# Optimization experiments

Hardware: AMD Instinct MI355X
Metric: run time of the kernel (lower is better)

The kernel has to match this reference:

```python
import jax, jax.numpy as jnp
import numpy as np

NUM_BINS = 10
HIST_RANGE = 10.0
LN_EPS = 1e-5
NUM_SERVERS = 64
START_IDX = 2 + 2 + NUM_SERVERS  # = 68


def layer_norm(x, g, b):
    mu = jnp.mean(x, axis=-1, keepdims=True)
    var = jnp.mean(jnp.square(x - mu), axis=-1, keepdims=True)
    return (x - mu) * jax.lax.rsqrt(var + LN_EPS) * g + b


def batched_histogram(w):
    # w: [B, S]; replicates np.histogram(w_i, bins=10, range=(0,10)) per row,
    # then normalizes by (sum + 1e-8). Values outside [0,10] are excluded;
    # value == 10 falls in the last bin.
    idx = jnp.clip(jnp.floor(w * (NUM_BINS / HIST_RANGE)).astype(jnp.int32), 0, NUM_BINS - 1)
    mask = ((w >= 0.0) & (w <= HIST_RANGE)).astype(w.dtype)
    oh = jax.nn.one_hot(idx, NUM_BINS, dtype=w.dtype) * mask[..., None]  # [B,S,NB]
    hist = jnp.sum(oh, axis=1)  # [B,NB]
    return hist / (jnp.sum(hist, axis=-1, keepdims=True) + 1e-8)


def setup_inputs() -> dict:
    key = jax.random.key(0)
    ks = jax.random.split(key, 16)
    B, OBS, ACT, H, NB = 65536, 512, 64, 128, NUM_BINS
    COMB = (OBS - NUM_SERVERS) + 128 + 64  # 640

    def lin(k, fin, fout):
        bound = 1.0 / np.sqrt(fin)
        kw, kb = jax.random.split(k)
        return (jax.random.uniform(kw, (fin, fout), jnp.float32, -bound, bound),
                jax.random.uniform(kb, (fout,), jnp.float32, -bound, bound))

    obs = jax.random.uniform(ks[0], (B, OBS), jnp.float32, 0.0, 10.0)
    preference = jax.random.uniform(ks[1], (B, 2), jnp.float32)
    h_w1, h_b1 = lin(ks[2], NB, H)
    h_w2, h_b2 = lin(ks[3], H, H)
    p_w, p_b = lin(ks[4], 2, 64)
    s_w1, s_b1 = lin(ks[5], COMB, 256)
    s_w2, s_b2 = lin(ks[6], 256, 256)
    qd_w, qd_b = lin(ks[7], 256, ACT)
    qe_w, qe_b = lin(ks[8], 256, ACT)
    return {
        'obs': obs, 'preference': preference,
        'h_w1': h_w1, 'h_b1': h_b1,
        'h_ln1_g': jnp.ones((H,)), 'h_ln1_b': jnp.zeros((H,)),
        'h_w2': h_w2, 'h_b2': h_b2,
        'h_ln2_g': jnp.ones((H,)), 'h_ln2_b': jnp.zeros((H,)),
        'p_w': p_w, 'p_b': p_b,
        'p_ln_g': jnp.ones((64,)), 'p_ln_b': jnp.zeros((64,)),
        's_w1': s_w1, 's_b1': s_b1,
        's_ln1_g': jnp.ones((256,)), 's_ln1_b': jnp.zeros((256,)),
        's_w2': s_w2, 's_b2': s_b2,
        's_ln2_g': jnp.ones((256,)), 's_ln2_b': jnp.zeros((256,)),
        'qd_w': qd_w, 'qd_b': qd_b, 'qe_w': qe_w, 'qe_b': qe_b,
    }


def reference(obs, preference,
              h_w1, h_b1, h_ln1_g, h_ln1_b, h_w2, h_b2, h_ln2_g, h_ln2_b,
              p_w, p_b, p_ln_g, p_ln_b,
              s_w1, s_b1, s_ln1_g, s_ln1_b, s_w2, s_b2, s_ln2_g, s_ln2_b,
              qd_w, qd_b, qe_w, qe_b):
    server_workloads = obs[:, START_IDX:START_IDX + NUM_SERVERS]
    obs_wo = jnp.concatenate([obs[:, :START_IDX], obs[:, START_IDX + NUM_SERVERS:]], axis=-1)

    hist = batched_histogram(server_workloads)  # [B, 10]
    h = layer_norm(jax.nn.relu(hist @ h_w1 + h_b1), h_ln1_g, h_ln1_b)
    h = layer_norm(jax.nn.relu(h @ h_w2 + h_b2), h_ln2_g, h_ln2_b)  # [B,128]

    p = layer_norm(jax.nn.relu(preference @ p_w + p_b), p_ln_g, p_ln_b)  # [B,64]

    combined = jnp.concatenate([obs_wo, h, p], axis=-1)  # [B,640]
    s = layer_norm(jax.nn.relu(combined @ s_w1 + s_b1), s_ln1_g, s_ln1_b)
    s = layer_norm(jax.nn.relu(s @ s_w2 + s_b2), s_ln2_g, s_ln2_b)  # [B,256]

    q_delay = s @ qd_w + qd_b   # [B,A]
    q_energy = s @ qe_w + qe_b  # [B,A]
    return jnp.stack([q_delay, q_energy], axis=-1)  # [B,A,2]
```

## Files before the change

kernel.cpp:

```cpp
#include <hip/hip_runtime.h>

typedef __bf16 bf16x8 __attribute__((ext_vector_type(8)));
typedef __bf16 bf16x4 __attribute__((ext_vector_type(4)));
typedef float  f32x4  __attribute__((ext_vector_type(4)));

#define OFF_W1  0
#define OFF_W2  163840
#define OFF_WQ  229376
#define OFF_WH1 262144
#define OFF_WH2 266240
#define WS_ELEMS 282624
#define CE_CH2 0
#define CE_EH2 128
#define CE_C2  256
#define CE_E2  512
#define CE_CQ  768
#define CE_EQ  896

__global__ __launch_bounds__(256) void prep_kernel(
    const float* __restrict__ s_w1, const float* __restrict__ s_w2,
    const float* __restrict__ qd_w, const float* __restrict__ qe_w,
    const float* __restrict__ h_w1, const float* __restrict__ h_w2,
    const float* __restrict__ h_g1, const float* __restrict__ s_g1,
    const float* __restrict__ s_g2,
    __bf16* __restrict__ wsb)
{
  int idx = blockIdx.x * 256 + threadIdx.x;
  if (idx >= WS_ELEMS) return;
  float val = 0.f;
  if (idx < OFF_W2) {
    int t = idx;
    int j = t & 7, l = (t >> 3) & 63, rest = t >> 9;
    int nt = rest & 15, ks = rest >> 4;
    int k = ks * 32 + (l >> 4) * 8 + j, n = nt * 16 + (l & 15);
    val = s_w1[k * 256 + n];
  } else if (idx < OFF_WQ) {
    int t = idx - OFF_W2;
    int j = t & 7, l = (t >> 3) & 63, rest = t >> 9;
    int nt = rest & 15, ks = rest >> 4;
    int k = ks * 32 + (l >> 4) * 8 + j, n = nt * 16 + (l & 15);
    val = s_w2[k * 256 + n] * s_g1[k];
  } else if (idx < OFF_WH1) {
    int t = idx - OFF_WQ;
    int j = t & 7, l = (t >> 3) & 63, rest = t >> 9;
    int nt = rest & 7, ks = rest >> 3;
    int k = ks * 32 + (l >> 4) * 8 + j, n = nt * 16 + (l & 15);
    int a = n >> 1;
    val = ((n & 1) ? qe_w[k * 64 + a] : qd_w[k * 64 + a]) * s_g2[k];
  } else if (idx < OFF_WH2) {
    int t = idx - OFF_WH1;
    int j = t & 7, l = (t >> 3) & 63, rest = t >> 9;
    int nt = rest & 7;
    int k = (l >> 4) * 8 + j, n = nt * 16 + (l & 15);
    val = (k < 10) ? h_w1[k * 128 + n] : 0.f;
  } else {
    int t = idx - OFF_WH2;
    int j = t & 7, l = (t >> 3) & 63, rest = t >> 9;
    int nt = rest & 7, ks = rest >> 3;
    int k = ks * 32 + (l >> 4) * 8 + j, n = nt * 16 + (l & 15);
    val = h_w2[k * 128 + n] * h_g1[k];
  }
  wsb[idx] = (__bf16)val;
}

__global__ __launch_bounds__(256) void prep_ce(
    const float* __restrict__ h_w2, const float* __restrict__ h_g1,
    const float* __restrict__ h_bb1, const float* __restrict__ h_b2,
    const float* __restrict__ s_w2, const float* __restrict__ s_g1,
    const float* __restrict__ s_bb1, const float* __restrict__ s_b2,
    const float* __restrict__ qd_w, const float* __restrict__ qe_w,
    const float* __restrict__ s_g2, const float* __restrict__ s_bb2,
    const float* __restrict__ qd_b, const float* __restrict__ qe_b,
    float* __restrict__ ce)
{
  int t = blockIdx.x * 256 + threadIdx.x;
  if (t < 128) {
    float s = 0.f;
    for (int k = 0; k < 128; ++k) s += h_g1[k] * h_w2[k * 128 + t];
    ce[CE_CH2 + t] = s;
  } else if (t < 256) {
    int n = t - 128;
    float s = h_b2[n];
    for (int k = 0; k < 128; ++k) s += h_bb1[k] * h_w2[k * 128 + n];
    ce[t] = s;
  } else if (t < 512) {
    int n = t - 256;
    float s = 0.f;
    for (int k = 0; k < 256; ++k) s += s_g1[k] * s_w2[k * 256 + n];
    ce[t] = s;
  } else if (t < 768) {
    int n = t - 512;
    float s = s_b2[n];
    for (int k = 0; k < 256; ++k) s += s_bb1[k] * s_w2[k * 256 + n];
    ce[t] = s;
  } else if (t < 896) {
    int n = t - 768, a = n >> 1;
    const float* W = (n & 1) ? qe_w : qd_w;
    float s = 0.f;
    for (int k = 0; k < 256; ++k) s += s_g2[k] * W[k * 64 + a];
    ce[t] = s;
  } else if (t < 1024) {
    int n = t - 896, a = n >> 1;
    const float* W = (n & 1) ? qe_w : qd_w;
    float s = (n & 1) ? qe_b[a] : qd_b[a];
    for (int k = 0; k < 256; ++k) s += s_bb2[k] * W[k * 64 + a];
    ce[t] = s;
  }
}

template<int CTRL>
__device__ __forceinline__ float dppadd(float x) {
  int p = __builtin_amdgcn_mov_dpp(__float_as_int(x), CTRL, 0xF, 0xF, true);
  return x + __int_as_float(p);
}
__device__ __forceinline__ float row16_reduce(float x) {
  x = dppadd<0x121>(x);
  x = dppadd<0x122>(x);
  x = dppadd<0x124>(x);
  x = dppadd<0x128>(x);
  return x;
}

__device__ __forceinline__ void slot_stats(const float* slot, float invW, int quad,
                                           float mu[4], float rs[4]) {
  f32x4 v0 = *(const f32x4*)(slot + quad * 8);
  f32x4 v1 = *(const f32x4*)(slot + quad * 8 + 4);
  float ts[4] = {v0[0], v0[2], v1[0], v1[2]};
  float tq[4] = {v0[1], v0[3], v1[1], v1[3]};
#pragma unroll
  for (int r = 0; r < 4; ++r) {
    mu[r] = ts[r] * invW;
    float var = tq[r] * invW - mu[r] * mu[r];
    rs[r] = rsqrtf(var + 1e-5f);
  }
}

template<int NTW>
__device__ __forceinline__ void reduce_slot(float x[NTW][4], float* slot, int lane) {
  const int quad = lane >> 4, ln = lane & 15;
  float s[4] = {0, 0, 0, 0}, q[4] = {0, 0, 0, 0};
#pragma unroll
  for (int i = 0; i < NTW; ++i)
#pragma unroll
    for (int r = 0; r < 4; ++r) { s[r] += x[i][r]; q[r] += x[i][r] * x[i][r]; }
#pragma unroll
  for (int r = 0; r < 4; ++r) { s[r] = row16_reduce(s[r]); q[r] = row16_reduce(q[r]); }
  if (ln == 0) {
#pragma unroll
    for (int r = 0; r < 4; ++r) {
      int m = quad * 4 + r;
      atomicAdd(&slot[2 * m], s[r]);
      atomicAdd(&slot[2 * m + 1], q[r]);
    }
  }
  __syncthreads();
}

template<int KSTEPS, int NT_TOT, int NTW>
__device__ __forceinline__ void run_gemm(const __bf16* A, int astride,
    const bf16x8* __restrict__ Bsw, int wave, int lane, f32x4 acc[NTW])
{
  const int quad = lane >> 4, ln = lane & 15;
  const int ntb = wave * NTW;
  bf16x8 bcur[NTW];
#pragma unroll
  for (int i = 0; i < NTW; ++i) bcur[i] = Bsw[(ntb + i) * 64 + lane];
#pragma unroll
  for (int ks = 0; ks < KSTEPS; ++ks) {
    bf16x8 bnxt[NTW];
    if (ks + 1 < KSTEPS) {
#pragma unroll
      for (int i = 0; i < NTW; ++i)
        bnxt[i] = Bsw[((ks + 1) * NT_TOT + ntb + i) * 64 + lane];
    }
    bf16x8 a = *(const bf16x8*)(A + ln * astride + ks * 32 + quad * 8);
#pragma unroll
    for (int i = 0; i < NTW; ++i)
      acc[i] = __builtin_amdgcn_mfma_f32_16x16x32_bf16(a, bcur[i], acc[i], 0, 0, 0);
    if (ks + 1 < KSTEPS) {
#pragma unroll
      for (int i = 0; i < NTW; ++i) bcur[i] = bnxt[i];
    }
  }
}

template<int NTW>
__device__ __forceinline__ void epilogue_raw(f32x4 acc[NTW],
    const float* __restrict__ bias,
    __bf16* Adst, int dstride, int dstcol0,
    float* slot, int wave, int lane)
{
  const int quad = lane >> 4, ln = lane & 15;
  float x[NTW][4];
#pragma unroll
  for (int i = 0; i < NTW; ++i) {
    int n = (wave * NTW + i) * 16 + ln;
    float b = bias[n];
#pragma unroll
    for (int r = 0; r < 4; ++r) {
      x[i][r] = fmaxf(acc[i][r] + b, 0.f);
      Adst[(quad * 4 + r) * dstride + dstcol0 + n] = (__bf16)x[i][r];
    }
  }
  reduce_slot<NTW>(x, slot, lane);
}

template<int NTW>
__device__ __forceinline__ void epilogue_fold_raw(f32x4 acc[NTW],
    const float* __restrict__ cvec, const float* __restrict__ evec,
    const float* __restrict__ slot_prev, float invWprev,
    __bf16* Adst, int dstride, int dstcol0,
    float* slot, int wave, int lane)
{
  const int quad = lane >> 4, ln = lane & 15;
  float mu[4], rs[4];
  slot_stats(slot_prev, invWprev, quad, mu, rs);
  float x[NTW][4];
#pragma unroll
  for (int i = 0; i < NTW; ++i) {
    int n = (wave * NTW + i) * 16 + ln;
    float c = cvec[n], e = evec[n];
#pragma unroll
    for (int r = 0; r < 4; ++r) {
      float z = fmaf(rs[r], fmaf(-mu[r], c, acc[i][r]), e);
      x[i][r] = fmaxf(z, 0.f);
      Adst[(quad * 4 + r) * dstride + dstcol0 + n] = (__bf16)x[i][r];
    }
  }
  reduce_slot<NTW>(x, slot, lane);
}

__global__ __launch_bounds__(512, 8) void critic_kernel(
    const float* __restrict__ obs, const float* __restrict__ pref,
    const float* __restrict__ h_b1,
    const float* __restrict__ h_g2, const float* __restrict__ h_bb2,
    const float* __restrict__ p_w, const float* __restrict__ p_b,
    const float* __restrict__ p_g, const float* __restrict__ p_bb,
    const float* __restrict__ s_b1,
    const __bf16* __restrict__ wsb, const float* __restrict__ ce,
    float* __restrict__ out)
{
  __shared__ __align__(16) __bf16 A_comb[16 * 648];
  __shared__ __align__(16) __bf16 A_s[16 * 264];
  __shared__ __align__(16) __bf16 A_h[16 * 40];
  __shared__ __align__(16) float red4[4][32];

  const int tid = threadIdx.x;
  const int wave = tid >> 6, lane = tid & 63;
  const int rowbase = blockIdx.x * 16;
  __bf16* X2 = A_comb;

  if (tid < 128) ((float*)red4)[tid] = 0.f;

  float pw0 = p_w[lane], pw1 = p_w[64 + lane], pb = p_b[lane];
  float pg = p_g[lane], pbb = p_bb[lane];
#pragma unroll
  for (int r = 0; r < 2; ++r) {
    int row = wave * 2 + r;
    int grow = rowbase + row;
    const float* orow = obs + (size_t)grow * 512;
#pragma unroll
    for (int j = 0; j < 2; ++j) {
      int l = lane + 64 * j;
      if (l < 112) {
        int src4 = (l < 17) ? l : l + 16;
        float4 v = *(const float4*)(orow + 4 * src4);
        bf16x4 o;
        o[0] = (__bf16)v.x; o[1] = (__bf16)v.y; o[2] = (__bf16)v.z; o[3] = (__bf16)v.w;
        *(bf16x4*)(&A_comb[row * 648 + 4 * l]) = o;
      }
    }
    float w = orow[68 + lane];
    int bi = (int)floorf(w);
    bi = bi < 0 ? 0 : (bi > 9 ? 9 : bi);
    bool valid = (w >= 0.f) && (w <= 10.f);
    float tot = 0.f, mine = 0.f;
#pragma unroll
    for (int b = 0; b < 10; ++b) {
      unsigned long long mk = __ballot(valid && (bi == b));
      float c = (float)__popcll(mk);
      tot += c;
      if (lane == b) mine = c;
    }
    float inv = 1.f / (tot + 1e-8f);
    if (lane < 32) A_h[row * 40 + lane] = (__bf16)((lane < 10) ? mine * inv : 0.f);
    float a0 = pref[grow * 2], a1 = pref[grow * 2 + 1];
    float v = fmaxf(fmaf(a0, pw0, fmaf(a1, pw1, pb)), 0.f);
    float s1 = v, s2 = v * v;
    s1 = row16_reduce(s1); s2 = row16_reduce(s2);
    s1 += __shfl_xor(s1, 16, 64); s2 += __shfl_xor(s2, 16, 64);
    s1 += __shfl_xor(s1, 32, 64); s2 += __shfl_xor(s2, 32, 64);
    float mu = s1 * (1.f / 64.f);
    float var = s2 * (1.f / 64.f) - mu * mu;
    float o = (v - mu) * rsqrtf(var + 1e-5f) * pg + pbb;
    A_comb[row * 648 + 576 + lane] = (__bf16)o;
  }
  __syncthreads();

  {
    f32x4 acc[1] = {};
    run_gemm<1, 8, 1>(A_h, 40, (const bf16x8*)(wsb + OFF_WH1), wave, lane, acc);
    epilogue_raw<1>(acc, h_b1, A_s, 264, 0, red4[0], wave, lane);
  }
  {
    f32x4 acc[1] = {};
    run_gemm<4, 8, 1>(A_s, 264, (const bf16x8*)(wsb + OFF_WH2), wave, lane, acc);
    const int quad = lane >> 4, ln = lane & 15;
    float mu0[4], rs0[4];
    slot_stats(red4[0], 1.f / 128.f, quad, mu0, rs0);
    int n = wave * 16 + ln;
    float c = ce[CE_CH2 + n], e = ce[CE_EH2 + n];
    float x[1][4];
#pragma unroll
    for (int r = 0; r < 4; ++r) {
      float z = fmaf(rs0[r], fmaf(-mu0[r], c, acc[0][r]), e);
      x[0][r] = fmaxf(z, 0.f);
    }
    reduce_slot<1>(x, red4[1], lane);
    float mu[4], rs[4];
    slot_stats(red4[1], 1.f / 128.f, quad, mu, rs);
    float gg = h_g2[n], bv = h_bb2[n];
#pragma unroll
    for (int r = 0; r < 4; ++r) {
      float o = (x[0][r] - mu[r]) * rs[r] * gg + bv;
      A_comb[(quad * 4 + r) * 648 + 448 + n] = (__bf16)o;
    }
    __syncthreads();
  }
  {
    f32x4 acc[2] = {};
    run_gemm<20, 16, 2>(A_comb, 648, (const bf16x8*)(wsb + OFF_W1), wave, lane, acc);
    epilogue_raw<2>(acc, s_b1, A_s, 264, 0, red4[2], wave, lane);
  }
  {
    f32x4 acc[2] = {};
    run_gemm<8, 16, 2>(A_s, 264, (const bf16x8*)(wsb + OFF_W2), wave, lane, acc);
    epilogue_fold_raw<2>(acc, ce + CE_C2, ce + CE_E2, red4[2], 1.f / 256.f,
                         X2, 264, 0, red4[3], wave, lane);
  }
  {
    f32x4 acc[1] = {};
    run_gemm<8, 8, 1>(X2, 264, (const bf16x8*)(wsb + OFF_WQ), wave, lane, acc);
    const int quad = lane >> 4, ln = lane & 15;
    float mu[4], rs[4];
    slot_stats(red4[3], 1.f / 256.f, quad, mu, rs);
    int n = wave * 16 + ln;
    float c = ce[CE_CQ + n], e = ce[CE_EQ + n];
#pragma unroll
    for (int r = 0; r < 4; ++r) {
      int m = quad * 4 + r;
      out[(size_t)(rowbase + m) * 128 + n] = fmaf(rs[r], fmaf(-mu[r], c, acc[0][r]), e);
    }
  }
}

extern "C" void kernel_launch(void* const* d_in, const int* in_sizes, int n_in,
                              void* d_out, int out_size, void* d_ws, size_t ws_size,
                              hipStream_t stream) {
  const float* obs    = (const float*)d_in[0];
  const float* pref   = (const float*)d_in[1];
  const float* h_w1   = (const float*)d_in[2];
  const float* h_b1   = (const float*)d_in[3];
  const float* h_g1   = (const float*)d_in[4];
  const float* h_bb1  = (const float*)d_in[5];
  const float* h_w2   = (const float*)d_in[6];
  const float* h_b2   = (const float*)d_in[7];
  const float* h_g2   = (const float*)d_in[8];
  const float* h_bb2  = (const float*)d_in[9];
  const float* p_w    = (const float*)d_in[10];
  const float* p_b    = (const float*)d_in[11];
  const float* p_g    = (const float*)d_in[12];
  const float* p_bb   = (const float*)d_in[13];
  const float* s_w1   = (const float*)d_in[14];
  const float* s_b1   = (const float*)d_in[15];
  const float* s_g1   = (const float*)d_in[16];
  const float* s_bb1  = (const float*)d_in[17];
  const float* s_w2   = (const float*)d_in[18];
  const float* s_b2   = (const float*)d_in[19];
  const float* s_g2   = (const float*)d_in[20];
  const float* s_bb2  = (const float*)d_in[21];
  const float* qd_w   = (const float*)d_in[22];
  const float* qd_b   = (const float*)d_in[23];
  const float* qe_w   = (const float*)d_in[24];
  const float* qe_b   = (const float*)d_in[25];

  __bf16* wsb = (__bf16*)d_ws;
  float* ce = (float*)(wsb + WS_ELEMS);
  int B = in_sizes[0] / 512;
  int nblocks = B / 16;

  prep_kernel<<<(WS_ELEMS + 255) / 256, 256, 0, stream>>>(
      s_w1, s_w2, qd_w, qe_w, h_w1, h_w2, h_g1, s_g1, s_g2, wsb);
  prep_ce<<<4, 256, 0, stream>>>(
      h_w2, h_g1, h_bb1, h_b2, s_w2, s_g1, s_bb1, s_b2,
      qd_w, qe_w, s_g2, s_bb2, qd_b, qe_b, ce);
  critic_kernel<<<nblocks, 512, 0, stream>>>(
      obs, pref, h_b1, h_g2, h_bb2, p_w, p_b, p_g, p_bb, s_b1,
      (const __bf16*)wsb, (const float*)ce, (float*)d_out);
}
```

Before: 346.5 us.

## Fold histogram LayerNorm2 into first trunk GEMM and merge prep kernels

Writes the un-normalised hidden activations straight into the combined buffer and folds the second histogram LayerNorm's gamma into the s_w1 rows. Its mean, rstd and beta are applied in the first trunk epilogue through precomputed column vectors, with the GEMM split into three K ranges so the hist segment gets its own accumulator. This removes a stats pass, a normalise-and-store pass and one __syncthreads. The two prep kernels are merged into one launch, and stats computation is hoisted before each GEMM. A barrier is dropped and floorf is replaced with truncation, which relies on the mask for negative values. The extra accumulators add register pressure.

```diff
diff --git a/kernel.cpp b/kernel.cpp
--- a/kernel.cpp
+++ b/kernel.cpp
@@ -16,17 +16,71 @@
 #define CE_E2  512
 #define CE_CQ  768
 #define CE_EQ  896
+#define CE_C1S 1024
+#define CE_E1S 1280
+#define CE_N   1536
 
 __global__ __launch_bounds__(256) void prep_kernel(
-    const float* __restrict__ s_w1, const float* __restrict__ s_w2,
+    const float* __restrict__ s_w1, const float* __restrict__ s_b1,
+    const float* __restrict__ s_w2, const float* __restrict__ s_b2,
     const float* __restrict__ qd_w, const float* __restrict__ qe_w,
+    const float* __restrict__ qd_b, const float* __restrict__ qe_b,
     const float* __restrict__ h_w1, const float* __restrict__ h_w2,
-    const float* __restrict__ h_g1, const float* __restrict__ s_g1,
-    const float* __restrict__ s_g2,
-    __bf16* __restrict__ wsb)
+    const float* __restrict__ h_b2,
+    const float* __restrict__ h_g1, const float* __restrict__ h_bb1,
+    const float* __restrict__ h_g2, const float* __restrict__ h_bb2,
+    const float* __restrict__ s_g1, const float* __restrict__ s_bb1,
+    const float* __restrict__ s_g2, const float* __restrict__ s_bb2,
+    __bf16* __restrict__ wsb, float* __restrict__ ce)
 {
   int idx = blockIdx.x * 256 + threadIdx.x;
-  if (idx >= WS_ELEMS) return;
+  if (idx >= WS_ELEMS) {
+    int t = idx - WS_ELEMS;
+    if (t >= CE_N) return;
+    if (t < 128) {
+      float s = 0.f;
+      for (int k = 0; k < 128; ++k) s += h_g1[k] * h_w2[k * 128 + t];
+      ce[CE_CH2 + t] = s;
+    } else if (t < 256) {
+      int n = t - 128;
+      float s = h_b2[n];
+      for (int k = 0; k < 128; ++k) s += h_bb1[k] * h_w2[k * 128 + n];
+      ce[t] = s;
+    } else if (t < 512) {
+      int n = t - 256;
+      float s = 0.f;
+      for (int k = 0; k < 256; ++k) s += s_g1[k] * s_w2[k * 256 + n];
+      ce[t] = s;
+    } else if (t < 768) {
+      int n = t - 512;
+      float s = s_b2[n];
+      for (int k = 0; k < 256; ++k) s += s_bb1[k] * s_w2[k * 256 + n];
+      ce[t] = s;
+    } else if (t < 896) {
+      int n = t - 768, a = n >> 1;
+      const float* W = (n & 1) ? qe_w : qd_w;
+      float s = 0.f;
+      for (int k = 0; k < 256; ++k) s += s_g2[k] * W[k * 64 + a];
+      ce[t] = s;
+    } else if (t < 1024) {
+      int n = t - 896, a = n >> 1;
+      const float* W = (n & 1) ? qe_w : qd_w;
+      float s = (n & 1) ? qe_b[a] : qd_b[a];
+      for (int k = 0; k < 256; ++k) s += s_bb2[k] * W[k * 64 + a];
+      ce[t] = s;
+    } else if (t < 1280) {
+      int n = t - 1024;
+      float s = 0.f;
+      for (int k = 0; k < 128; ++k) s += h_g2[k] * s_w1[(448 + k) * 256 + n];
+      ce[t] = s;
+    } else {
+      int n = t - 1280;
+      float s = s_b1[n];
+      for (int k = 0; k < 128; ++k) s += h_bb2[k] * s_w1[(448 + k) * 256 + n];
+      ce[t] = s;
+    }
+    return;
+  }
   float val = 0.f;
   if (idx < OFF_W2) {
     int t = idx;
@@ -34,6 +88,7 @@
     int nt = rest & 15, ks = rest >> 4;
     int k = ks * 32 + (l >> 4) * 8 + j, n = nt * 16 + (l & 15);
     val = s_w1[k * 256 + n];
+    if (k >= 448 && k < 576) val *= h_g2[k - 448];
   } else if (idx < OFF_WQ) {
     int t = idx - OFF_W2;
     int j = t & 7, l = (t >> 3) & 63, rest = t >> 9;
@@ -63,51 +118,6 @@
   wsb[idx] = (__bf16)val;
 }
 
-__global__ __launch_bounds__(256) void prep_ce(
-    const float* __restrict__ h_w2, const float* __restrict__ h_g1,
-    const float* __restrict__ h_bb1, const float* __restrict__ h_b2,
-    const float* __restrict__ s_w2, const float* __restrict__ s_g1,
-    const float* __restrict__ s_bb1, const float* __restrict__ s_b2,
-    const float* __restrict__ qd_w, const float* __restrict__ qe_w,
-    const float* __restrict__ s_g2, const float* __restrict__ s_bb2,
-    const float* __restrict__ qd_b, const float* __restrict__ qe_b,
-    float* __restrict__ ce)
-{
-  int t = blockIdx.x * 256 + threadIdx.x;
-  if (t < 128) {
-    float s = 0.f;
-    for (int k = 0; k < 128; ++k) s += h_g1[k] * h_w2[k * 128 + t];
-    ce[CE_CH2 + t] = s;
-  } else if (t < 256) {
-    int n = t - 128;
-    float s = h_b2[n];
-    for (int k = 0; k < 128; ++k) s += h_bb1[k] * h_w2[k * 128 + n];
-    ce[t] = s;
-  } else if (t < 512) {
-    int n = t - 256;
-    float s = 0.f;
-    for (int k = 0; k < 256; ++k) s += s_g1[k] * s_w2[k * 256 + n];
-    ce[t] = s;
-  } else if (t < 768) {
-    int n = t - 512;
-    float s = s_b2[n];
-    for (int k = 0; k < 256; ++k) s += s_bb1[k] * s_w2[k * 256 + n];
-    ce[t] = s;
-  } else if (t < 896) {
-    int n = t - 768, a = n >> 1;
-    const float* W = (n & 1) ? qe_w : qd_w;
-    float s = 0.f;
-    for (int k = 0; k < 256; ++k) s += s_g2[k] * W[k * 64 + a];
-    ce[t] = s;
-  } else if (t < 1024) {
-    int n = t - 896, a = n >> 1;
-    const float* W = (n & 1) ? qe_w : qd_w;
-    float s = (n & 1) ? qe_b[a] : qd_b[a];
-    for (int k = 0; k < 256; ++k) s += s_bb2[k] * W[k * 64 + a];
-    ce[t] = s;
-  }
-}
-
 template<int CTRL>
 __device__ __forceinline__ float dppadd(float x) {
   int p = __builtin_amdgcn_mov_dpp(__float_as_int(x), CTRL, 0xF, 0xF, true);
@@ -205,38 +215,11 @@
   reduce_slot<NTW>(x, slot, lane);
 }
 
-template<int NTW>
-__device__ __forceinline__ void epilogue_fold_raw(f32x4 acc[NTW],
-    const float* __restrict__ cvec, const float* __restrict__ evec,
-    const float* __restrict__ slot_prev, float invWprev,
-    __bf16* Adst, int dstride, int dstcol0,
-    float* slot, int wave, int lane)
-{
-  const int quad = lane >> 4, ln = lane & 15;
-  float mu[4], rs[4];
-  slot_stats(slot_prev, invWprev, quad, mu, rs);
-  float x[NTW][4];
-#pragma unroll
-  for (int i = 0; i < NTW; ++i) {
-    int n = (wave * NTW + i) * 16 + ln;
-    float c = cvec[n], e = evec[n];
-#pragma unroll
-    for (int r = 0; r < 4; ++r) {
-      float z = fmaf(rs[r], fmaf(-mu[r], c, acc[i][r]), e);
-      x[i][r] = fmaxf(z, 0.f);
-      Adst[(quad * 4 + r) * dstride + dstcol0 + n] = (__bf16)x[i][r];
-    }
-  }
-  reduce_slot<NTW>(x, slot, lane);
-}
-
 __global__ __launch_bounds__(512, 8) void critic_kernel(
     const float* __restrict__ obs, const float* __restrict__ pref,
     const float* __restrict__ h_b1,
-    const float* __restrict__ h_g2, const float* __restrict__ h_bb2,
     const float* __restrict__ p_w, const float* __restrict__ p_b,
     const float* __restrict__ p_g, const float* __restrict__ p_bb,
-    const float* __restrict__ s_b1,
     const __bf16* __restrict__ wsb, const float* __restrict__ ce,
     float* __restrict__ out)
 {
@@ -247,6 +230,7 @@
 
   const int tid = threadIdx.x;
   const int wave = tid >> 6, lane = tid & 63;
+  const int quad = lane >> 4, ln = lane & 15;
   const int rowbase = blockIdx.x * 16;
   __bf16* X2 = A_comb;
 
@@ -271,7 +255,7 @@
       }
     }
     float w = orow[68 + lane];
-    int bi = (int)floorf(w);
+    int bi = (int)w;
     bi = bi < 0 ? 0 : (bi > 9 ? 9 : bi);
     bool valid = (w >= 0.f) && (w <= 10.f);
     float tot = 0.f, mine = 0.f;
@@ -303,11 +287,10 @@
     epilogue_raw<1>(acc, h_b1, A_s, 264, 0, red4[0], wave, lane);
   }
   {
+    float mu0[4], rs0[4];
+    slot_stats(red4[0], 1.f / 128.f, quad, mu0, rs0);
     f32x4 acc[1] = {};
     run_gemm<4, 8, 1>(A_s, 264, (const bf16x8*)(wsb + OFF_WH2), wave, lane, acc);
-    const int quad = lane >> 4, ln = lane & 15;
-    float mu0[4], rs0[4];
-    slot_stats(red4[0], 1.f / 128.f, quad, mu0, rs0);
     int n = wave * 16 + ln;
     float c = ce[CE_CH2 + n], e = ce[CE_EH2 + n];
     float x[1][4];
@@ -315,41 +298,64 @@
     for (int r = 0; r < 4; ++r) {
       float z = fmaf(rs0[r], fmaf(-mu0[r], c, acc[0][r]), e);
       x[0][r] = fmaxf(z, 0.f);
+      A_comb[(quad * 4 + r) * 648 + 448 + n] = (__bf16)x[0][r];
     }
     reduce_slot<1>(x, red4[1], lane);
-    float mu[4], rs[4];
-    slot_stats(red4[1], 1.f / 128.f, quad, mu, rs);
-    float gg = h_g2[n], bv = h_bb2[n];
-#pragma unroll
-    for (int r = 0; r < 4; ++r) {
-      float o = (x[0][r] - mu[r]) * rs[r] * gg + bv;
-      A_comb[(quad * 4 + r) * 648 + 448 + n] = (__bf16)o;
-    }
-    __syncthreads();
   }
   {
-    f32x4 acc[2] = {};
-    run_gemm<20, 16, 2>(A_comb, 648, (const bf16x8*)(wsb + OFF_W1), wave, lane, acc);
-    epilogue_raw<2>(acc, s_b1, A_s, 264, 0, red4[2], wave, lane);
+    float mu1[4], rs1[4];
+    slot_stats(red4[1], 1.f / 128.f, quad, mu1, rs1);
+    const bf16x8* B1 = (const bf16x8*)(wsb + OFF_W1);
+    f32x4 accM[2] = {};
+    f32x4 accS[2] = {};
+    run_gemm<14, 16, 2>(A_comb, 648, B1, wave, lane, accM);
+    run_gemm<4, 16, 2>(A_comb + 448, 648, B1 + 14 * 16 * 64, wave, lane, accS);
+    run_gemm<2, 16, 2>(A_comb + 576, 648, B1 + 18 * 16 * 64, wave, lane, accM);
+    float x[2][4];
+#pragma unroll
+    for (int i = 0; i < 2; ++i) {
+      int n = (wave * 2 + i) * 16 + ln;
+      float c = ce[CE_C1S + n], e = ce[CE_E1S + n];
+#pragma unroll
+      for (int r = 0; r < 4; ++r) {
+        float t = fmaf(-mu1[r] * rs1[r], c, e);
+        float z = accM[i][r] + fmaf(rs1[r], accS[i][r], t);
+        x[i][r] = fmaxf(z, 0.f);
+        A_s[(quad * 4 + r) * 264 + n] = (__bf16)x[i][r];
+      }
+    }
+    reduce_slot<2>(x, red4[2], lane);
   }
   {
+    float mu2[4], rs2[4];
+    slot_stats(red4[2], 1.f / 256.f, quad, mu2, rs2);
     f32x4 acc[2] = {};
     run_gemm<8, 16, 2>(A_s, 264, (const bf16x8*)(wsb + OFF_W2), wave, lane, acc);
-    epilogue_fold_raw<2>(acc, ce + CE_C2, ce + CE_E2, red4[2], 1.f / 256.f,
-                         X2, 264, 0, red4[3], wave, lane);
+    float x[2][4];
+#pragma unroll
+    for (int i = 0; i < 2; ++i) {
+      int n = (wave * 2 + i) * 16 + ln;
+      float c = ce[CE_C2 + n], e = ce[CE_E2 + n];
+#pragma unroll
+      for (int r = 0; r < 4; ++r) {
+        float z = fmaf(rs2[r], fmaf(-mu2[r], c, acc[i][r]), e);
+        x[i][r] = fmaxf(z, 0.f);
+        X2[(quad * 4 + r) * 264 + n] = (__bf16)x[i][r];
+      }
+    }
+    reduce_slot<2>(x, red4[3], lane);
   }
   {
+    float mu3[4], rs3[4];
+    slot_stats(red4[3], 1.f / 256.f, quad, mu3, rs3);
     f32x4 acc[1] = {};
     run_gemm<8, 8, 1>(X2, 264, (const bf16x8*)(wsb + OFF_WQ), wave, lane, acc);
-    const int quad = lane >> 4, ln = lane & 15;
-    float mu[4], rs[4];
-    slot_stats(red4[3], 1.f / 256.f, quad, mu, rs);
     int n = wave * 16 + ln;
     float c = ce[CE_CQ + n], e = ce[CE_EQ + n];
 #pragma unroll
     for (int r = 0; r < 4; ++r) {
       int m = quad * 4 + r;
-      out[(size_t)(rowbase + m) * 128 + n] = fmaf(rs[r], fmaf(-mu[r], c, acc[0][r]), e);
+      out[(size_t)(rowbase + m) * 128 + n] = fmaf(rs3[r], fmaf(-mu3[r], c, acc[0][r]), e);
     }
   }
 }
@@ -389,12 +395,11 @@
   int B = in_sizes[0] / 512;
   int nblocks = B / 16;
 
-  prep_kernel<<<(WS_ELEMS + 255) / 256, 256, 0, stream>>>(
-      s_w1, s_w2, qd_w, qe_w, h_w1, h_w2, h_g1, s_g1, s_g2, wsb);
-  prep_ce<<<4, 256, 0, stream>>>(
-      h_w2, h_g1, h_bb1, h_b2, s_w2, s_g1, s_bb1, s_b2,
-      qd_w, qe_w, s_g2, s_bb2, qd_b, qe_b, ce);
+  prep_kernel<<<(WS_ELEMS + CE_N + 255) / 256, 256, 0, stream>>>(
+      s_w1, s_b1, s_w2, s_b2, qd_w, qe_w, qd_b, qe_b,
+      h_w1, h_w2, h_b2, h_g1, h_bb1, h_g2, h_bb2,
+      s_g1, s_bb1, s_g2, s_bb2, wsb, ce);
   critic_kernel<<<nblocks, 512, 0, stream>>>(
-      obs, pref, h_b1, h_g2, h_bb2, p_w, p_b, p_g, p_bb, s_b1,
+      obs, pref, h_b1, p_w, p_b, p_g, p_bb,
       (const __bf16*)wsb, (const float*)ce, (float*)d_out);
 }
```

New measurement: 372.2 us. +7.4%, slower.
